# Kernel tuning notes

Hardware: AMD Instinct MI355X
Metric: run time of the kernel (lower is better)

Reference implementation:

```python
import jax, jax.numpy as jnp
import numpy as np

N, D, L, OUT, E = 50000, 64, 3, 16, 800000


def setup_inputs() -> dict:
    key = jax.random.key(0)
    ks = jax.random.split(key, 7)
    F = jax.random.normal(ks[0], (N, D), dtype=jnp.float32)
    src = jax.random.randint(ks[1], (E,), 0, N, dtype=jnp.int32)
    dst = jax.random.randint(ks[2], (E,), 0, N, dtype=jnp.int32)
    gcn_w = jax.random.normal(ks[3], (L, D, D), dtype=jnp.float32) / np.float32(np.sqrt(D))
    gcn_b = jnp.zeros((L, D), dtype=jnp.float32)
    fc_w = jax.random.normal(ks[4], (OUT, N * D), dtype=jnp.float32) / np.float32(np.sqrt(N * D))
    fc_b = jnp.zeros((OUT,), dtype=jnp.float32)
    return {"F": F, "src": src, "dst": dst, "gcn_w": gcn_w, "gcn_b": gcn_b,
            "fc_w": fc_w, "fc_b": fc_b}


def reference(F, src, dst, gcn_w, gcn_b, fc_w, fc_b):
    n = F.shape[0]
    # dgl.add_self_loop: append a self edge for every node
    loops = jnp.arange(n, dtype=src.dtype)
    s = jnp.concatenate([src, loops])
    d = jnp.concatenate([dst, loops])
    ones = jnp.ones(s.shape[0], dtype=F.dtype)
    deg_out = jax.ops.segment_sum(ones, s, num_segments=n)  # out-degree of src
    deg_in = jax.ops.segment_sum(ones, d, num_segments=n)   # in-degree of dst
    # self loops guarantee deg >= 1
    norm_src = deg_out ** -0.5
    norm_dst = deg_in ** -0.5
    x = F
    for i in range(gcn_w.shape[0]):
        h = x * norm_src[:, None]                              # [N, D]
        agg = jax.ops.segment_sum(h[s], d, num_segments=n)     # SpMM gather-scatter
        x = (agg * norm_dst[:, None]) @ gcn_w[i] + gcn_b[i]    # GraphConv norm='both'
        x = jax.nn.relu(x)
    flat = jax.nn.relu(x.reshape(-1))                          # Flatten(start_dim=0) + ReLU
    return fc_w @ flat + fc_b                                  # [OUT]
```

## Files before the change

### kernel.cpp

```cpp
#include <hip/hip_runtime.h>
#include <cstdint>

#define Nn 50000
#define Dd 64
#define Ee 800000
#define NBLK 196
#define FC_BLOCKS 512
#define ND4 (Nn*Dd/4)

__device__ __forceinline__ float relu_f(float v){ return v > 0.f ? v : 0.f; }

__device__ __forceinline__ unsigned short f2bf(float f){
    unsigned u = __float_as_uint(f);
    u += 0x7fffu + ((u >> 16) & 1u);
    return (unsigned short)(u >> 16);
}
__device__ __forceinline__ void add_bf8(float* a, uint4 u){
    a[0] += __uint_as_float(u.x << 16);
    a[1] += __uint_as_float(u.x & 0xffff0000u);
    a[2] += __uint_as_float(u.y << 16);
    a[3] += __uint_as_float(u.y & 0xffff0000u);
    a[4] += __uint_as_float(u.z << 16);
    a[5] += __uint_as_float(u.z & 0xffff0000u);
    a[6] += __uint_as_float(u.w << 16);
    a[7] += __uint_as_float(u.w & 0xffff0000u);
}

__global__ __launch_bounds__(256) void k_degree(const int* __restrict__ src, const int* __restrict__ dst,
                                                unsigned* __restrict__ dout, unsigned* __restrict__ din){
    int e = blockIdx.x * 256 + threadIdx.x;
    if (e < Ee){
        atomicAdd(&dout[src[e]], 1u);
        atomicAdd(&din[dst[e]], 1u);
    }
}

__global__ __launch_bounds__(256) void k_norms(const unsigned* __restrict__ dout, const unsigned* __restrict__ din,
                                               float* __restrict__ ns, float* __restrict__ nd){
    int i = blockIdx.x * 256 + threadIdx.x;
    if (i < Nn){
        ns[i] = rsqrtf((float)(dout[i] + 1u));
        nd[i] = rsqrtf((float)(din[i] + 1u));
    }
}

__global__ __launch_bounds__(256) void k_blocksum(const unsigned* __restrict__ din, unsigned* __restrict__ bsum){
    __shared__ unsigned s[256];
    int t = threadIdx.x; int i = blockIdx.x * 256 + t;
    s[t] = (i < Nn) ? din[i] : 0u;
    __syncthreads();
    for (int off = 128; off > 0; off >>= 1){ if (t < off) s[t] += s[t + off]; __syncthreads(); }
    if (t == 0) bsum[blockIdx.x] = s[0];
}

__global__ __launch_bounds__(256) void k_scanblocks(const unsigned* __restrict__ bsum, unsigned* __restrict__ boff,
                                                    unsigned* __restrict__ offsets){
    __shared__ unsigned s[256];
    int t = threadIdx.x;
    unsigned v = (t < NBLK) ? bsum[t] : 0u;
    s[t] = v; __syncthreads();
    for (int off = 1; off < 256; off <<= 1){
        unsigned add = (t >= off) ? s[t - off] : 0u;
        __syncthreads();
        s[t] += add;
        __syncthreads();
    }
    boff[t] = s[t] - v;
    if (t == 255) offsets[Nn] = s[255];
}

__global__ __launch_bounds__(256) void k_offsets(const unsigned* __restrict__ din, const unsigned* __restrict__ boff,
                                                 unsigned* __restrict__ offsets, unsigned* __restrict__ cursor){
    __shared__ unsigned s[256];
    int t = threadIdx.x; int i = blockIdx.x * 256 + t;
    unsigned v = (i < Nn) ? din[i] : 0u;
    s[t] = v; __syncthreads();
    for (int off = 1; off < 256; off <<= 1){
        unsigned add = (t >= off) ? s[t - off] : 0u;
        __syncthreads();
        s[t] += add;
        __syncthreads();
    }
    if (i < Nn){
        unsigned val = s[t] - v + boff[blockIdx.x];
        offsets[i] = val;
        cursor[i]  = val;
    }
}

__global__ __launch_bounds__(256) void k_fillcsr(const int* __restrict__ src, const int* __restrict__ dst,
                                                 unsigned* __restrict__ cursor, unsigned* __restrict__ csr){
    int e = blockIdx.x * 256 + threadIdx.x;
    if (e < Ee){
        unsigned pos = atomicAdd(&cursor[dst[e]], 1u);
        csr[pos] = (unsigned)src[e];
    }
}

__global__ __launch_bounds__(256) void k_h0(const float* __restrict__ x, const float* __restrict__ ns,
                                            unsigned short* __restrict__ h){
    int i = blockIdx.x * 256 + threadIdx.x;
    const float4* x4 = (const float4*)x;
    float s = ns[i >> 4];
    float4 v = x4[i];
    ushort4 o;
    o.x = f2bf(v.x * s); o.y = f2bf(v.y * s);
    o.z = f2bf(v.z * s); o.w = f2bf(v.w * s);
    ((ushort4*)h)[i] = o;
}

__global__ __launch_bounds__(256) void k_gather(const unsigned short* __restrict__ h,
                                                const unsigned* __restrict__ offsets,
                                                const unsigned* __restrict__ csr, const float* __restrict__ nd,
                                                float* __restrict__ agg){
    int v = blockIdx.x * 4 + (threadIdx.x >> 6);
    int lane = threadIdx.x & 63;
    int slot = lane >> 3;
    int sub  = lane & 7;
    const uint4* h16 = (const uint4*)h;

    float acc[8];
    #pragma unroll
    for (int i = 0; i < 8; i++) acc[i] = 0.f;

    unsigned beg = offsets[v], end = offsets[v + 1];

    if (slot == 0){
        add_bf8(acc, h16[(size_t)v * 8 + sub]);
    }

    unsigned e = beg + slot;
    for (; e + 8 < end; e += 16){
        int s0 = (int)csr[e];
        int s1 = (int)csr[e + 8];
        uint4 u0 = h16[(size_t)s0 * 8 + sub];
        uint4 u1 = h16[(size_t)s1 * 8 + sub];
        add_bf8(acc, u0);
        add_bf8(acc, u1);
    }
    if (e < end){
        add_bf8(acc, h16[(size_t)((int)csr[e]) * 8 + sub]);
    }

    #pragma unroll
    for (int i = 0; i < 8; i++) acc[i] += __shfl_xor(acc[i], 8, 64);
    #pragma unroll
    for (int i = 0; i < 8; i++) acc[i] += __shfl_xor(acc[i], 16, 64);
    #pragma unroll
    for (int i = 0; i < 8; i++) acc[i] += __shfl_xor(acc[i], 32, 64);

    if (slot == 0){
        float s = nd[v];
        float4* aggp = (float4*)agg;
        float4 o0 = make_float4(acc[0] * s, acc[1] * s, acc[2] * s, acc[3] * s);
        float4 o1 = make_float4(acc[4] * s, acc[5] * s, acc[6] * s, acc[7] * s);
        aggp[(size_t)v * 16 + sub * 2 + 0] = o0;
        aggp[(size_t)v * 16 + sub * 2 + 1] = o1;
    }
}

__global__ __launch_bounds__(256) void k_gemm(const float* __restrict__ agg, const float* __restrict__ W,
                                              const float* __restrict__ bias, const float* __restrict__ ns,
                                              void* __restrict__ xout, int bf16_prescale_out){
    __shared__ float As[64 * 65];
    __shared__ float Ws[64 * 64];
    int t = threadIdx.x;
    int m_base = blockIdx.x * 64;
    const float4* W4   = (const float4*)W;
    float4* Ws4        = (float4*)Ws;
    const float4* agg4 = (const float4*)agg;
    #pragma unroll
    for (int i = 0; i < 4; i++){
        int g = t + 256 * i;
        Ws4[g] = W4[g];
        int m = g >> 4, q = g & 15;
        int node = m_base + m;
        float4 v = make_float4(0.f, 0.f, 0.f, 0.f);
        if (node < Nn) v = agg4[node * 16 + q];
        float* dp = &As[m * 65 + q * 4];
        dp[0] = v.x; dp[1] = v.y; dp[2] = v.z; dp[3] = v.w;
    }
    __syncthreads();
    int tm = t >> 4, tn = t & 15;
    float acc[4][4];
    #pragma unroll
    for (int i = 0; i < 4; i++)
        #pragma unroll
        for (int j = 0; j < 4; j++) acc[i][j] = 0.f;
    #pragma unroll 4
    for (int k = 0; k < 64; k++){
        float4 w = *(const float4*)&Ws[k * 64 + tn * 4];
        float a[4];
        #pragma unroll
        for (int i = 0; i < 4; i++) a[i] = As[(tm * 4 + i) * 65 + k];
        #pragma unroll
        for (int i = 0; i < 4; i++){
            acc[i][0] += a[i] * w.x;
            acc[i][1] += a[i] * w.y;
            acc[i][2] += a[i] * w.z;
            acc[i][3] += a[i] * w.w;
        }
    }
    float4 b4 = ((const float4*)bias)[tn];
    #pragma unroll
    for (int i = 0; i < 4; i++){
        int node = m_base + tm * 4 + i;
        if (node < Nn){
            float4 r;
            r.x = relu_f(acc[i][0] + b4.x);
            r.y = relu_f(acc[i][1] + b4.y);
            r.z = relu_f(acc[i][2] + b4.z);
            r.w = relu_f(acc[i][3] + b4.w);
            if (bf16_prescale_out){
                float s = ns[node];
                ushort4 o;
                o.x = f2bf(r.x * s); o.y = f2bf(r.y * s);
                o.z = f2bf(r.z * s); o.w = f2bf(r.w * s);
                ((ushort4*)xout)[node * 16 + tn] = o;
            } else {
                ((float4*)xout)[node * 16 + tn] = r;
            }
        }
    }
}

__global__ __launch_bounds__(256) void k_fc(const float* __restrict__ fcw, const float* __restrict__ x,
                                            float* __restrict__ partials){
    int t = threadIdx.x;
    const float4* x4 = (const float4*)x;
    const float4* w4 = (const float4*)fcw;
    float p[16];
    #pragma unroll
    for (int o = 0; o < 16; o++) p[o] = 0.f;
    for (int i = blockIdx.x * 256 + t; i < ND4; i += FC_BLOCKS * 256){
        float4 xv = x4[i];
        #pragma unroll
        for (int o = 0; o < 16; o++){
            float4 wv = w4[(size_t)o * ND4 + i];
            p[o] += wv.x * xv.x + wv.y * xv.y + wv.z * xv.z + wv.w * xv.w;
        }
    }
    #pragma unroll
    for (int o = 0; o < 16; o++){
        for (int off = 32; off > 0; off >>= 1) p[o] += __shfl_down(p[o], off, 64);
    }
    __shared__ float red[4][16];
    int lane = t & 63, wid = t >> 6;
    if (lane == 0){
        #pragma unroll
        for (int o = 0; o < 16; o++) red[wid][o] = p[o];
    }
    __syncthreads();
    if (t < 16) partials[blockIdx.x * 16 + t] = red[0][t] + red[1][t] + red[2][t] + red[3][t];
}

__global__ __launch_bounds__(256) void k_fc2(const float* __restrict__ partials, const float* __restrict__ fcb,
                                             float* __restrict__ out){
    __shared__ float red[256];
    int t = threadIdx.x; int o = t & 15, j0 = t >> 4;
    float s = 0.f;
    for (int j = j0; j < FC_BLOCKS; j += 16) s += partials[j * 16 + o];
    red[t] = s; __syncthreads();
    for (int off = 128; off >= 16; off >>= 1){ if (t < off) red[t] += red[t + off]; __syncthreads(); }
    if (t < 16) out[t] = red[t] + fcb[t];
}

extern "C" void kernel_launch(void* const* d_in, const int* in_sizes, int n_in,
                              void* d_out, int out_size, void* d_ws, size_t ws_size,
                              hipStream_t stream) {
    const float* F     = (const float*)d_in[0];
    const int*   src   = (const int*)d_in[1];
    const int*   dst   = (const int*)d_in[2];
    const float* gcn_w = (const float*)d_in[3];
    const float* gcn_b = (const float*)d_in[4];
    const float* fc_w  = (const float*)d_in[5];
    const float* fc_b  = (const float*)d_in[6];
    float* out = (float*)d_out;

    char* wsp = (char*)d_ws;
    auto alloc = [&](size_t bytes) -> char* {
        char* p = wsp;
        wsp += (bytes + 255) & ~size_t(255);
        return p;
    };
    unsigned* deg      = (unsigned*)alloc(2 * Nn * 4);
    unsigned* deg_out_ = deg;
    unsigned* deg_in_  = deg + Nn;
    unsigned* offsets  = (unsigned*)alloc((Nn + 1) * 4);
    unsigned* cursor   = (unsigned*)alloc(Nn * 4);
    unsigned* bsum     = (unsigned*)alloc(256 * 4);
    unsigned* boff     = (unsigned*)alloc(256 * 4);
    unsigned* csr      = (unsigned*)alloc(Ee * 4);
    float* norm_src    = (float*)alloc(Nn * 4);
    float* norm_dst    = (float*)alloc(Nn * 4);
    float* partials    = (float*)alloc(FC_BLOCKS * 16 * 4);
    unsigned short* hA = (unsigned short*)alloc((size_t)Nn * 64 * 2);
    unsigned short* hB = (unsigned short*)alloc((size_t)Nn * 64 * 2);
    float* aggb        = (float*)alloc((size_t)Nn * 64 * 4);
    float* xf          = (float*)alloc((size_t)Nn * 64 * 4);

    hipMemsetAsync(deg, 0, 2 * Nn * 4, stream);

    k_degree<<<Ee / 256, 256, 0, stream>>>(src, dst, deg_out_, deg_in_);
    k_norms<<<NBLK, 256, 0, stream>>>(deg_out_, deg_in_, norm_src, norm_dst);
    k_blocksum<<<NBLK, 256, 0, stream>>>(deg_in_, bsum);
    k_scanblocks<<<1, 256, 0, stream>>>(bsum, boff, offsets);
    k_offsets<<<NBLK, 256, 0, stream>>>(deg_in_, boff, offsets, cursor);
    k_fillcsr<<<Ee / 256, 256, 0, stream>>>(src, dst, cursor, csr);

    k_h0<<<ND4 / 256, 256, 0, stream>>>(F, norm_src, hA);

    int nblk_gemm = (Nn + 63) / 64;
    k_gather<<<Nn / 4, 256, 0, stream>>>(hA, offsets, csr, norm_dst, aggb);
    k_gemm<<<nblk_gemm, 256, 0, stream>>>(aggb, gcn_w + 0 * 4096, gcn_b + 0 * 64, norm_src, hB, 1);
    k_gather<<<Nn / 4, 256, 0, stream>>>(hB, offsets, csr, norm_dst, aggb);
    k_gemm<<<nblk_gemm, 256, 0, stream>>>(aggb, gcn_w + 1 * 4096, gcn_b + 1 * 64, norm_src, hA, 1);
    k_gather<<<Nn / 4, 256, 0, stream>>>(hA, offsets, csr, norm_dst, aggb);
    k_gemm<<<nblk_gemm, 256, 0, stream>>>(aggb, gcn_w + 2 * 4096, gcn_b + 2 * 64, norm_src, xf, 0);

    k_fc<<<FC_BLOCKS, 256, 0, stream>>>(fc_w, xf, partials);
    k_fc2<<<1, 256, 0, stream>>>(partials, fc_b, out);
}
```

Before: 546.7 us.

## Fuse gather, per-node GEMM and FC into per-layer kernels

After: 580.4 us. 1.06x slower.

```diff
diff --git a/kernel.cpp b/kernel.cpp
--- a/kernel.cpp
+++ b/kernel.cpp
@@ -5,8 +5,8 @@
 #define Dd 64
 #define Ee 800000
 #define NBLK 196
-#define FC_BLOCKS 512
 #define ND4 (Nn*Dd/4)
+#define NDTOT ((size_t)Nn * 64)
 
 __device__ __forceinline__ float relu_f(float v){ return v > 0.f ? v : 0.f; }
 
@@ -35,19 +35,17 @@
     }
 }
 
-__global__ __launch_bounds__(256) void k_norms(const unsigned* __restrict__ dout, const unsigned* __restrict__ din,
-                                               float* __restrict__ ns, float* __restrict__ nd){
-    int i = blockIdx.x * 256 + threadIdx.x;
+__global__ __launch_bounds__(256) void k_blocksum(const unsigned* __restrict__ din, const unsigned* __restrict__ dout,
+                                                  unsigned* __restrict__ bsum,
+                                                  float* __restrict__ ns, float* __restrict__ nd){
+    __shared__ unsigned s[256];
+    int t = threadIdx.x; int i = blockIdx.x * 256 + t;
+    unsigned v = (i < Nn) ? din[i] : 0u;
+    s[t] = v;
     if (i < Nn){
         ns[i] = rsqrtf((float)(dout[i] + 1u));
-        nd[i] = rsqrtf((float)(din[i] + 1u));
-    }
-}
-
-__global__ __launch_bounds__(256) void k_blocksum(const unsigned* __restrict__ din, unsigned* __restrict__ bsum){
-    __shared__ unsigned s[256];
-    int t = threadIdx.x; int i = blockIdx.x * 256 + t;
-    s[t] = (i < Nn) ? din[i] : 0u;
+        nd[i] = rsqrtf((float)(v + 1u));
+    }
     __syncthreads();
     for (int off = 128; off > 0; off >>= 1){ if (t < off) s[t] += s[t + off]; __syncthreads(); }
     if (t == 0) bsum[blockIdx.x] = s[0];
@@ -109,12 +107,12 @@
     ((ushort4*)h)[i] = o;
 }
 
-__global__ __launch_bounds__(256) void k_gather(const unsigned short* __restrict__ h,
-                                                const unsigned* __restrict__ offsets,
-                                                const unsigned* __restrict__ csr, const float* __restrict__ nd,
-                                                float* __restrict__ agg){
-    int v = blockIdx.x * 4 + (threadIdx.x >> 6);
-    int lane = threadIdx.x & 63;
+__device__ __forceinline__ float layer_body(const unsigned short* __restrict__ h,
+                                            const unsigned* __restrict__ offsets,
+                                            const unsigned* __restrict__ csr,
+                                            const float* __restrict__ nd,
+                                            const float* __restrict__ bias,
+                                            const float* Ws, int v, int lane){
     int slot = lane >> 3;
     int sub  = lane & 7;
     const uint4* h16 = (const uint4*)h;
@@ -149,117 +147,104 @@
     #pragma unroll
     for (int i = 0; i < 8; i++) acc[i] += __shfl_xor(acc[i], 32, 64);
 
-    if (slot == 0){
-        float s = nd[v];
-        float4* aggp = (float4*)agg;
-        float4 o0 = make_float4(acc[0] * s, acc[1] * s, acc[2] * s, acc[3] * s);
-        float4 o1 = make_float4(acc[4] * s, acc[5] * s, acc[6] * s, acc[7] * s);
-        aggp[(size_t)v * 16 + sub * 2 + 0] = o0;
-        aggp[(size_t)v * 16 + sub * 2 + 1] = o1;
-    }
-}
-
-__global__ __launch_bounds__(256) void k_gemm(const float* __restrict__ agg, const float* __restrict__ W,
-                                              const float* __restrict__ bias, const float* __restrict__ ns,
-                                              void* __restrict__ xout, int bf16_prescale_out){
-    __shared__ float As[64 * 65];
-    __shared__ float Ws[64 * 64];
+    float ndv = nd[v];
+    #pragma unroll
+    for (int i = 0; i < 8; i++) acc[i] *= ndv;
+
+    float y = bias[lane];
+    #pragma unroll
+    for (int c = 0; c < 8; c++){
+        #pragma unroll
+        for (int i = 0; i < 8; i++){
+            float a = __shfl(acc[i], c, 64);
+            y = fmaf(a, Ws[(c * 8 + i) * 64 + lane], y);
+        }
+    }
+    return y;
+}
+
+__global__ __launch_bounds__(256) void k_layer01(const unsigned short* __restrict__ hin,
+                                                 const unsigned* __restrict__ offsets,
+                                                 const unsigned* __restrict__ csr,
+                                                 const float* __restrict__ nd, const float* __restrict__ ns,
+                                                 const float* __restrict__ W, const float* __restrict__ bias,
+                                                 unsigned short* __restrict__ hout){
+    __shared__ float Ws[4096];
     int t = threadIdx.x;
-    int m_base = blockIdx.x * 64;
-    const float4* W4   = (const float4*)W;
-    float4* Ws4        = (float4*)Ws;
-    const float4* agg4 = (const float4*)agg;
-    #pragma unroll
-    for (int i = 0; i < 4; i++){
-        int g = t + 256 * i;
-        Ws4[g] = W4[g];
-        int m = g >> 4, q = g & 15;
-        int node = m_base + m;
-        float4 v = make_float4(0.f, 0.f, 0.f, 0.f);
-        if (node < Nn) v = agg4[node * 16 + q];
-        float* dp = &As[m * 65 + q * 4];
-        dp[0] = v.x; dp[1] = v.y; dp[2] = v.z; dp[3] = v.w;
-    }
-    __syncthreads();
-    int tm = t >> 4, tn = t & 15;
-    float acc[4][4];
-    #pragma unroll
-    for (int i = 0; i < 4; i++)
+    {
+        const float4* W4 = (const float4*)W;
+        float4* Ws4 = (float4*)Ws;
         #pragma unroll
-        for (int j = 0; j < 4; j++) acc[i][j] = 0.f;
-    #pragma unroll 4
-    for (int k = 0; k < 64; k++){
-        float4 w = *(const float4*)&Ws[k * 64 + tn * 4];
-        float a[4];
+        for (int i = 0; i < 4; i++) Ws4[t + 256 * i] = W4[t + 256 * i];
+    }
+    __syncthreads();
+    int v = blockIdx.x * 4 + (t >> 6);
+    int lane = t & 63;
+    float y = layer_body(hin, offsets, csr, nd, bias, Ws, v, lane);
+    y = relu_f(y);
+    hout[(size_t)v * 64 + lane] = f2bf(y * ns[v]);
+}
+
+__global__ __launch_bounds__(256) void k_layer2fc(const unsigned short* __restrict__ hin,
+                                                  const unsigned* __restrict__ offsets,
+                                                  const unsigned* __restrict__ csr,
+                                                  const float* __restrict__ nd,
+                                                  const float* __restrict__ W, const float* __restrict__ bias,
+                                                  const float* __restrict__ fcw,
+                                                  float* __restrict__ partials){
+    __shared__ float Ws[4096];
+    int t = threadIdx.x;
+    {
+        const float4* W4 = (const float4*)W;
+        float4* Ws4 = (float4*)Ws;
         #pragma unroll
-        for (int i = 0; i < 4; i++) a[i] = As[(tm * 4 + i) * 65 + k];
-        #pragma unroll
-        for (int i = 0; i < 4; i++){
-            acc[i][0] += a[i] * w.x;
-            acc[i][1] += a[i] * w.y;
-            acc[i][2] += a[i] * w.z;
-            acc[i][3] += a[i] * w.w;
-        }
-    }
-    float4 b4 = ((const float4*)bias)[tn];
-    #pragma unroll
-    for (int i = 0; i < 4; i++){
-        int node = m_base + tm * 4 + i;
-        if (node < Nn){
-            float4 r;
-            r.x = relu_f(acc[i][0] + b4.x);
-            r.y = relu_f(acc[i][1] + b4.y);
-            r.z = relu_f(acc[i][2] + b4.z);
-            r.w = relu_f(acc[i][3] + b4.w);
-            if (bf16_prescale_out){
-                float s = ns[node];
-                ushort4 o;
-                o.x = f2bf(r.x * s); o.y = f2bf(r.y * s);
-                o.z = f2bf(r.z * s); o.w = f2bf(r.w * s);
-                ((ushort4*)xout)[node * 16 + tn] = o;
-            } else {
-                ((float4*)xout)[node * 16 + tn] = r;
-            }
-        }
-    }
-}
-
-__global__ __launch_bounds__(256) void k_fc(const float* __restrict__ fcw, const float* __restrict__ x,
-                                            float* __restrict__ partials){
-    int t = threadIdx.x;
-    const float4* x4 = (const float4*)x;
-    const float4* w4 = (const float4*)fcw;
+        for (int i = 0; i < 4; i++) Ws4[t + 256 * i] = W4[t + 256 * i];
+    }
+    __syncthreads();
+    int v = blockIdx.x * 4 + (t >> 6);
+    int lane = t & 63;
+    float y = layer_body(hin, offsets, csr, nd, bias, Ws, v, lane);
+    y = relu_f(y);
+
     float p[16];
-    #pragma unroll
-    for (int o = 0; o < 16; o++) p[o] = 0.f;
-    for (int i = blockIdx.x * 256 + t; i < ND4; i += FC_BLOCKS * 256){
-        float4 xv = x4[i];
-        #pragma unroll
-        for (int o = 0; o < 16; o++){
-            float4 wv = w4[(size_t)o * ND4 + i];
-            p[o] += wv.x * xv.x + wv.y * xv.y + wv.z * xv.z + wv.w * xv.w;
-        }
-    }
-    #pragma unroll
-    for (int o = 0; o < 16; o++){
-        for (int off = 32; off > 0; off >>= 1) p[o] += __shfl_down(p[o], off, 64);
-    }
-    __shared__ float red[4][16];
-    int lane = t & 63, wid = t >> 6;
-    if (lane == 0){
-        #pragma unroll
-        for (int o = 0; o < 16; o++) red[wid][o] = p[o];
-    }
-    __syncthreads();
-    if (t < 16) partials[blockIdx.x * 16 + t] = red[0][t] + red[1][t] + red[2][t] + red[3][t];
-}
-
-__global__ __launch_bounds__(256) void k_fc2(const float* __restrict__ partials, const float* __restrict__ fcb,
-                                             float* __restrict__ out){
+    size_t col = (size_t)v * 64 + lane;
+    #pragma unroll
+    for (int o = 0; o < 16; o++) p[o] = y * fcw[(size_t)o * NDTOT + col];
+
+    __syncthreads();
+    #pragma unroll
+    for (int o = 0; o < 16; o++) Ws[o * 256 + t] = p[o];
+    __syncthreads();
+
+    int o = t >> 4, i = t & 15;
+    float s = 0.f;
+    #pragma unroll
+    for (int m = 0; m < 16; m++) s += Ws[o * 256 + m * 16 + i];
+    s += __shfl_down(s, 8, 64);
+    s += __shfl_down(s, 4, 64);
+    s += __shfl_down(s, 2, 64);
+    s += __shfl_down(s, 1, 64);
+    if (i == 0) partials[blockIdx.x * 16 + o] = s;
+}
+
+__global__ __launch_bounds__(256) void k_fc2a(const float* __restrict__ partials, float* __restrict__ part2){
     __shared__ float red[256];
-    int t = threadIdx.x; int o = t & 15, j0 = t >> 4;
+    int t = threadIdx.x; int o = t & 15, rr = t >> 4;
     float s = 0.f;
-    for (int j = j0; j < FC_BLOCKS; j += 16) s += partials[j * 16 + o];
+    for (int r = blockIdx.x * 16 + rr; r < 12500; r += 1024)
+        s += partials[r * 16 + o];
+    red[t] = s; __syncthreads();
+    for (int off = 128; off >= 16; off >>= 1){ if (t < off) red[t] += red[t + off]; __syncthreads(); }
+    if (t < 16) part2[blockIdx.x * 16 + t] = red[t];
+}
+
+__global__ __launch_bounds__(256) void k_fc2b(const float* __restrict__ part2, const float* __restrict__ fcb,
+                                              float* __restrict__ out){
+    __shared__ float red[256];
+    int t = threadIdx.x; int o = t & 15, g = t >> 4;
+    float s = 0.f;
+    #pragma unroll
+    for (int m = 0; m < 4; m++) s += part2[(g + 16 * m) * 16 + o];
     red[t] = s; __syncthreads();
     for (int off = 128; off >= 16; off >>= 1){ if (t < off) red[t] += red[t + off]; __syncthreads(); }
     if (t < 16) out[t] = red[t] + fcb[t];
@@ -293,31 +278,28 @@
     unsigned* csr      = (unsigned*)alloc(Ee * 4);
     float* norm_src    = (float*)alloc(Nn * 4);
     float* norm_dst    = (float*)alloc(Nn * 4);
-    float* partials    = (float*)alloc(FC_BLOCKS * 16 * 4);
-    unsigned short* hA = (unsigned short*)alloc((size_t)Nn * 64 * 2);
-    unsigned short* hB = (unsigned short*)alloc((size_t)Nn * 64 * 2);
-    float* aggb        = (float*)alloc((size_t)Nn * 64 * 4);
-    float* xf          = (float*)alloc((size_t)Nn * 64 * 4);
+    float* partials    = (float*)alloc(12500 * 16 * 4);
+    float* part2       = (float*)alloc(64 * 16 * 4);
+    unsigned short* hA = (unsigned short*)alloc(NDTOT * 2);
+    unsigned short* hB = (unsigned short*)alloc(NDTOT * 2);
 
     hipMemsetAsync(deg, 0, 2 * Nn * 4, stream);
 
     k_degree<<<Ee / 256, 256, 0, stream>>>(src, dst, deg_out_, deg_in_);
-    k_norms<<<NBLK, 256, 0, stream>>>(deg_out_, deg_in_, norm_src, norm_dst);
-    k_blocksum<<<NBLK, 256, 0, stream>>>(deg_in_, bsum);
+    k_blocksum<<<NBLK, 256, 0, stream>>>(deg_in_, deg_out_, bsum, norm_src, norm_dst);
     k_scanblocks<<<1, 256, 0, stream>>>(bsum, boff, offsets);
     k_offsets<<<NBLK, 256, 0, stream>>>(deg_in_, boff, offsets, cursor);
     k_fillcsr<<<Ee / 256, 256, 0, stream>>>(src, dst, cursor, csr);
 
     k_h0<<<ND4 / 256, 256, 0, stream>>>(F, norm_src, hA);
 
-    int nblk_gemm = (Nn + 63) / 64;
-    k_gather<<<Nn / 4, 256, 0, stream>>>(hA, offsets, csr, norm_dst, aggb);
-    k_gemm<<<nblk_gemm, 256, 0, stream>>>(aggb, gcn_w + 0 * 4096, gcn_b + 0 * 64, norm_src, hB, 1);
-    k_gather<<<Nn / 4, 256, 0, stream>>>(hB, offsets, csr, norm_dst, aggb);
-    k_gemm<<<nblk_gemm, 256, 0, stream>>>(aggb, gcn_w + 1 * 4096, gcn_b + 1 * 64, norm_src, hA, 1);
-    k_gather<<<Nn / 4, 256, 0, stream>>>(hA, offsets, csr, norm_dst, aggb);
-    k_gemm<<<nblk_gemm, 256, 0, stream>>>(aggb, gcn_w + 2 * 4096, gcn_b + 2 * 64, norm_src, xf, 0);
-
-    k_fc<<<FC_BLOCKS, 256, 0, stream>>>(fc_w, xf, partials);
-    k_fc2<<<1, 256, 0, stream>>>(partials, fc_b, out);
-}
+    k_layer01<<<Nn / 4, 256, 0, stream>>>(hA, offsets, csr, norm_dst, norm_src,
+                                          gcn_w + 0 * 4096, gcn_b + 0 * 64, hB);
+    k_layer01<<<Nn / 4, 256, 0, stream>>>(hB, offsets, csr, norm_dst, norm_src,
+                                          gcn_w + 1 * 4096, gcn_b + 1 * 64, hA);
+    k_layer2fc<<<Nn / 4, 256, 0, stream>>>(hA, offsets, csr, norm_dst,
+                                           gcn_w + 2 * 4096, gcn_b + 2 * 64, fc_w, partials);
+
+    k_fc2a<<<64, 256, 0, stream>>>(partials, part2);
+    k_fc2b<<<1, 256, 0, stream>>>(part2, fc_b, out);
+}
```
